# Performance work log

Hardware: AMD Instinct MI355X
Metric: run time of the kernel (lower is better)

## Reference

```python
import jax, jax.numpy as jnp
import numpy as np

B, C, T, H, W = 2, 256, 16, 32, 32
NH = 8
GROUPS = 32
EPS = 1e-6


def setup_inputs() -> dict:
    key = jax.random.key(0)
    ks = jax.random.split(key, 10)
    r = lambda k, shape: jax.random.normal(k, shape, dtype=jnp.float32) * 0.02
    return dict(
        x=jax.random.normal(ks[0], (B, C, T, H, W), dtype=jnp.float32),
        gn_gamma=jnp.ones((C,), jnp.float32),
        gn_beta=jnp.zeros((C,), jnp.float32),
        wq_s=r(ks[1], (C, C)), bq_s=jnp.zeros((C,), jnp.float32),
        wk_s=r(ks[2], (C, C)), bk_s=jnp.zeros((C,), jnp.float32),
        wv_s=r(ks[3], (C, C)), bv_s=jnp.zeros((C,), jnp.float32),
        wo_s=r(ks[4], (C, C)), bo_s=jnp.zeros((C,), jnp.float32),
        wq_t=r(ks[5], (C, C)),
        wk_t=r(ks[6], (C, C)),
        wv_t=r(ks[7], (C, C)),
        wf_t=r(ks[8], (C, C)), bf_t=jnp.zeros((C,), jnp.float32),
    )


def group_norm(x, gamma, beta):
    # x: (N, C, H, W), GroupNorm(32, eps=1e-6, affine)
    n, c, h, w = x.shape
    xg = x.reshape(n, GROUPS, c // GROUPS, h, w)
    mu = xg.mean(axis=(2, 3, 4), keepdims=True)
    var = xg.var(axis=(2, 3, 4), keepdims=True)
    xg = (xg - mu) * jax.lax.rsqrt(var + EPS)
    return xg.reshape(n, c, h, w) * gamma[None, :, None, None] + beta[None, :, None, None]


def spatial_attention(x, gn_gamma, gn_beta, wq, bq, wk, bk, wv, bv, wo, bo):
    # ldm SpatialSelfAttention: norm -> 1x1 conv q/k/v -> full HW self-attn -> 1x1 proj -> residual
    n, c, h, w = x.shape
    hf = group_norm(x, gn_gamma, gn_beta).reshape(n, c, h * w)  # (N, C, HW)
    q = jnp.einsum('oc,bcn->bno', wq, hf) + bq                  # (N, HW, C)
    k = jnp.einsum('oc,bcn->bon', wk, hf) + bk[None, :, None]   # (N, C, HW)
    v = jnp.einsum('oc,bcn->bon', wv, hf) + bv[None, :, None]   # (N, C, HW)
    attn = jax.nn.softmax(jnp.einsum('bic,bcj->bij', q, k) * (c ** -0.5), axis=-1)  # (N, HW, HW)
    out = jnp.einsum('bcj,bij->bci', v, attn)                   # (N, C, HW)
    out = jnp.einsum('oc,bcn->bon', wo, out) + bo[None, :, None]
    return x + out.reshape(n, c, h, w)


def axial_temporal_attention(x, wq, wk, wv, wf, bf):
    # x: (B, T, H, W, C); VideoGPT MultiHeadAttention with AxialAttention over T (axial_dim=-4)
    b, t, h, w, c = x.shape
    dk = c // NH

    def heads(y):  # (B,T,H,W,C) -> (B,H,W,NH,T,dk)
        return jnp.transpose(y.reshape(b, t, h, w, NH, dk), (0, 2, 3, 4, 1, 5))

    q = heads(x @ wq)
    k = heads(x @ wk)
    v = heads(x @ wv)
    scores = jnp.einsum('bhwntd,bhwnsd->bhwnts', q, k) / jnp.sqrt(jnp.float32(dk))
    attn = jax.nn.softmax(scores, axis=-1)
    out = jnp.einsum('bhwnts,bhwnsd->bhwntd', attn, v)          # (B,H,W,NH,T,dk)
    out = jnp.transpose(out, (0, 4, 1, 2, 3, 5)).reshape(b, t, h, w, c)
    return out @ wf + bf


def reference(x, gn_gamma, gn_beta, wq_s, bq_s, wk_s, bk_s, wv_s, bv_s, wo_s, bo_s,
              wq_t, wk_t, wv_t, wf_t, bf_t):
    b, c, t, h, w = x.shape
    # spatial branch: torch does a raw reshape (B,C,T,H,W)->(B*T,C,H,W); replicate exactly
    s = spatial_attention(x.reshape(b * t, c, h, w), gn_gamma, gn_beta,
                          wq_s, bq_s, wk_s, bk_s, wv_s, bv_s, wo_s, bo_s)
    s = s.reshape(b, c, t, h, w)
    # temporal branch: channels-last, axial attention over T
    xt = jnp.moveaxis(x, 1, -1)                                 # (B,T,H,W,C)
    tt = axial_temporal_attention(xt, wq_t, wk_t, wv_t, wf_t, bf_t)
    return s + jnp.moveaxis(tt, -1, 1)
```

## Files before the change

kernel.cpp:

```cpp
#include <hip/hip_runtime.h>
#include <stdint.h>

typedef uint16_t u16;
typedef __attribute__((ext_vector_type(8))) short s8v;
typedef __attribute__((ext_vector_type(4))) float f32x4;
typedef __attribute__((ext_vector_type(16))) float f32x16;
typedef __attribute__((ext_vector_type(4))) unsigned short us4;
typedef __attribute__((ext_vector_type(4))) unsigned int u32x4;

__device__ __forceinline__ float bf2f(u16 u) {
  union { uint32_t i; float f; } x; x.i = ((uint32_t)u) << 16; return x.f;
}
__device__ __forceinline__ u16 f2bf(float f) {
  union { float f; uint32_t i; } x; x.f = f;
  uint32_t r = (x.i + 0x7FFFu + ((x.i >> 16) & 1u)) >> 16;
  return (u16)r;
}
__device__ __forceinline__ uint32_t cvtpk(float a, float b) {
  uint32_t r;
  asm("v_cvt_pk_bf16_f32 %0, %1, %2" : "=v"(r) : "v"(a), "v"(b));
  return r;
}
__device__ __forceinline__ void gl2lds16(const u16* g, u16* l) {
  __builtin_amdgcn_global_load_lds(
      (const __attribute__((address_space(1))) uint32_t*)g,
      (__attribute__((address_space(3))) uint32_t*)l, 16, 0, 0);
}

__global__ __launch_bounds__(256) void gn_stats_kernel(const float* __restrict__ x,
                                                       float2* __restrict__ stats) {
  const int tid = threadIdx.x;
  const float* p = x + (long)blockIdx.x * 8192;
  float s = 0.f, s2 = 0.f;
#pragma unroll
  for (int it = 0; it < 8; ++it) {
    float4 v = *(const float4*)(p + it * 1024 + tid * 4);
    s  += v.x + v.y + v.z + v.w;
    s2 += v.x * v.x + v.y * v.y + v.z * v.z + v.w * v.w;
  }
#pragma unroll
  for (int off = 32; off >= 1; off >>= 1) {
    s  += __shfl_down(s, off);
    s2 += __shfl_down(s2, off);
  }
  __shared__ float ps[4], ps2[4];
  const int wv = tid >> 6, lane = tid & 63;
  if (lane == 0) { ps[wv] = s; ps2[wv] = s2; }
  __syncthreads();
  if (tid == 0) {
    float S1 = ps[0] + ps[1] + ps[2] + ps[3];
    float S2 = ps2[0] + ps2[1] + ps2[2] + ps2[3];
    float mean = S1 * (1.f / 8192.f);
    float var = S2 * (1.f / 8192.f) - mean * mean;
    stats[blockIdx.x] = make_float2(mean, rsqrtf(var + 1e-6f));
  }
}

__global__ __launch_bounds__(256) void wprep_kernel(
    const float* __restrict__ s0, const float* __restrict__ s1,
    const float* __restrict__ s2, const float* __restrict__ s3,
    const float* __restrict__ s4, const float* __restrict__ s5,
    const float* __restrict__ s6, const float* __restrict__ s7,
    u16* __restrict__ wbf) {
  const int mat = blockIdx.x, rb = blockIdx.y;
  const float* src = mat==0?s0:mat==1?s1:mat==2?s2:mat==3?s3:mat==4?s4:mat==5?s5:mat==6?s6:s7;
  u16* dst = wbf + mat * 65536 + rb * 16384;
  const int tid = threadIdx.x;
  if (mat < 4) {
    const float* sb = src + rb * 16384;
#pragma unroll
    for (int it = 0; it < 16; ++it) {
      int idx = it * 256 + tid;
      float4 v = *(const float4*)(sb + idx * 4);
      us4 o; o[0]=f2bf(v.x); o[1]=f2bf(v.y); o[2]=f2bf(v.z); o[3]=f2bf(v.w);
      *(us4*)(dst + idx * 4) = o;
    }
  } else {
    __shared__ u16 tl[64][264];
#pragma unroll
    for (int it = 0; it < 16; ++it) {
      int idx = it * 256 + tid;
      int c = idx >> 4, o4 = idx & 15;
      float4 v = *(const float4*)(src + c * 256 + rb * 64 + o4 * 4);
      tl[o4*4+0][c] = f2bf(v.x);
      tl[o4*4+1][c] = f2bf(v.y);
      tl[o4*4+2][c] = f2bf(v.z);
      tl[o4*4+3][c] = f2bf(v.w);
    }
    __syncthreads();
#pragma unroll
    for (int it = 0; it < 16; ++it) {
      int idx = it * 256 + tid;
      int o = idx >> 6, c4 = idx & 63;
      us4 u;
#pragma unroll
      for (int j = 0; j < 4; ++j) u[j] = tl[o][c4*4+j];
      *(us4*)(dst + o * 256 + c4 * 4) = u;
    }
  }
}

__global__ __launch_bounds__(512) void qkvst_kernel(
    const float* __restrict__ x, const float2* __restrict__ stats,
    const float* __restrict__ gamma, const float* __restrict__ beta,
    const u16* __restrict__ wbf,
    const float* __restrict__ bq, const float* __restrict__ bk, const float* __restrict__ bv,
    u16* __restrict__ qb, u16* __restrict__ kb, u16* __restrict__ vb,
    u16* __restrict__ qt, u16* __restrict__ kt, u16* __restrict__ vt) {
  __shared__ float gas[256], bes[256];
  __shared__ u16 ALDS[128 * 256];
  __shared__ u16 WLDS[2][64 * 256];
  const int bid = blockIdx.x;
  const int b = bid >> 7, st = bid & 127;
  const int s0 = st * 128;
  const int tt = s0 >> 10;
  const int n = b * 16 + tt;
  const int p0 = s0 & 1023;
  const long bbase = (long)b * 4194304;
  const long nbase = (long)n * 262144;
  const int tid = threadIdx.x, w = tid >> 6, lane = tid & 63;
  const int lhi = lane >> 4, llo = lane & 15;

  if (tid < 256) {
    float2 stv = stats[n * 32 + (tid >> 3)];
    float ga = gamma[tid] * stv.y;
    gas[tid] = ga;
    bes[tid] = beta[tid] - stv.x * ga;
  }
  const float* xb = x + bbase + s0;
#pragma unroll
  for (int it = 0; it < 16; ++it) {
    int idx = it * 512 + tid;
    int p = idx & 127, c4 = idx >> 7;
    us4 o;
#pragma unroll
    for (int j = 0; j < 4; ++j)
      o[j] = f2bf(xb[(long)(c4 * 4 + j) * 16384 + p]);
    int ch = c4 >> 1;
    *(us4*)&ALDS[p * 256 + ((ch ^ (p & 7)) << 3) + ((c4 & 1) << 2)] = o;
  }
  __syncthreads();
  const int arow = w * 16 + llo;
  s8v ar[8], ag[8];
#pragma unroll
  for (int kk = 0; kk < 8; ++kk)
    ar[kk] = *(const s8v*)&ALDS[arow * 256 + (((kk * 4 + lhi) ^ (arow & 7)) << 3)];
#pragma unroll
  for (int kk = 0; kk < 8; ++kk) {
    const int cb = kk * 32 + lhi * 8;
    s8v gg;
#pragma unroll
    for (int j = 0; j < 8; ++j)
      gg[j] = (short)f2bf(bf2f((u16)ar[kk][j]) * gas[cb + j] + bes[cb + j]);
    ag[kk] = gg;
  }

  auto stageW4 = [&](int t, int bu) {
    const int mat = (t < 12) ? (t >> 2) : (4 + ((t - 12) >> 2));
    const int sub = (t < 12) ? (t & 3) : ((t - 12) & 3);
    const u16* wsrc = wbf + mat * 65536 + (long)sub * 16384;
#pragma unroll
    for (int ii = 0; ii < 4; ++ii) {
      int s = ii * 512 + tid;
      int row = s >> 5, ch = s & 31;
      gl2lds16(wsrc + row * 256 + ((ch ^ (row & 7)) << 3), &WLDS[bu][s * 8]);
    }
  };

  stageW4(0, 0);
  __syncthreads();

  u16* vtl = ALDS;
  for (int t = 0; t < 24; ++t) {
    const int cur = t & 1;
    if (t < 23) stageW4(t + 1, cur ^ 1);
    f32x4 acc[4] = {};
    if (t < 12) {
#pragma unroll
      for (int kk = 0; kk < 8; ++kk)
#pragma unroll
        for (int nf = 0; nf < 4; ++nf) {
          int row = nf * 16 + llo;
          s8v bfr = *(const s8v*)&WLDS[cur][row * 256 + (((kk * 4 + lhi) ^ (row & 7)) << 3)];
          acc[nf] = __builtin_amdgcn_mfma_f32_16x16x32_bf16(ag[kk], bfr, acc[nf], 0, 0, 0);
        }
    } else {
#pragma unroll
      for (int kk = 0; kk < 8; ++kk)
#pragma unroll
        for (int nf = 0; nf < 4; ++nf) {
          int row = nf * 16 + llo;
          s8v bfr = *(const s8v*)&WLDS[cur][row * 256 + (((kk * 4 + lhi) ^ (row & 7)) << 3)];
          acc[nf] = __builtin_amdgcn_mfma_f32_16x16x32_bf16(ar[kk], bfr, acc[nf], 0, 0, 0);
        }
    }
    const int o0 = ((t < 12) ? (t & 3) : ((t - 12) & 3)) * 64;
    if (t < 8) {
      u16* dstb = (t < 4) ? qb : kb;
      const float* bias = (t < 4) ? bq : bk;
#pragma unroll
      for (int nf = 0; nf < 4; ++nf) {
        int o = o0 + nf * 16 + llo;
        float b_ = bias[o];
#pragma unroll
        for (int r = 0; r < 4; ++r)
          dstb[nbase + (long)(p0 + w * 16 + lhi * 4 + r) * 256 + o] = f2bf(acc[nf][r] + b_);
      }
    } else if (t < 12) {
#pragma unroll
      for (int nf = 0; nf < 4; ++nf) {
        int o = nf * 16 + llo;
        float b_ = bv[o0 + o];
#pragma unroll
        for (int r = 0; r < 4; ++r)
          vtl[o * 136 + w * 16 + lhi * 4 + r] = f2bf(acc[nf][r] + b_);
      }
      __syncthreads();
#pragma unroll
      for (int ii = 0; ii < 4; ++ii) {
        int i = ii * 512 + tid;
        int o = i >> 5, p4 = (i & 31) * 4;
        us4 u;
#pragma unroll
        for (int j = 0; j < 4; ++j) u[j] = vtl[o * 136 + p4 + j];
        *(us4*)(vb + nbase + (long)(o0 + o) * 1024 + p0 + p4) = u;
      }
    } else {
      u16* dstb = (t < 16) ? qt : (t < 20) ? kt : vt;
#pragma unroll
      for (int nf = 0; nf < 4; ++nf) {
        int o = o0 + nf * 16 + llo;
#pragma unroll
        for (int r = 0; r < 4; ++r)
          dstb[bbase + (long)(s0 + w * 16 + lhi * 4 + r) * 256 + o] = f2bf(acc[nf][r]);
      }
    }
    __syncthreads();
  }
}

__global__ __launch_bounds__(256, 1) void flash_kernel(const u16* __restrict__ qb,
                                                       const u16* __restrict__ kb,
                                                       const u16* __restrict__ vb,
                                                       u16* __restrict__ attb) {
  const int wg = blockIdx.x;
  const int swz = (wg & 7) * 64 + (wg >> 3);
  const int n = swz >> 4, qt = swz & 15;
  const int tid = threadIdx.x, w = tid >> 6, lane = tid & 63;
  const int q5 = lane & 31, h = lane >> 5;
  const int wq = w & 1;
  const int kh = w >> 1;
  const long nbase = (long)n * 262144;

  __shared__ u16 Kb[64 * 256];
  __shared__ u16 Vb[256 * 64];
  __shared__ float2 mlbuf[64];

  const int qrow = qt * 64 + wq * 32 + q5;
  const u16* qr = qb + nbase + (long)qrow * 256 + h * 8;
  s8v qa[16];
#pragma unroll
  for (int kk = 0; kk < 16; ++kk) qa[kk] = *(const s8v*)(qr + kk * 16);

  f32x16 oaccT[8] = {};
  float m_ = -3.4e38f, l_ = 0.f;
  constexpr float CEXP = 0.09016844f;

  auto stageKV = [&](int jt2) {
    const u16* kbase = kb + nbase + (long)jt2 * 16384;
    const u16* vbase = vb + nbase + (long)jt2 * 64;
#pragma unroll
    for (int ii = 0; ii < 8; ++ii) {
      int s = ii * 256 + tid;
      int row = s >> 5, ch = s & 31;
      gl2lds16(kbase + (long)row * 256 + ((ch ^ (row & 7)) << 3), &Kb[s * 8]);
    }
#pragma unroll
    for (int ii = 0; ii < 8; ++ii) {
      int s = ii * 256 + tid;
      int c = s >> 3, ch = s & 7;
      gl2lds16(vbase + (long)c * 1024 + ((ch ^ (c & 7)) << 3), &Vb[s * 8]);
    }
  };

  const int krow = kh * 32 + q5;
  for (int jt = 0; jt < 16; ++jt) {
    stageKV(jt);
    __syncthreads();

    f32x16 sacc = {};
    __builtin_amdgcn_s_setprio(1);
#pragma unroll
    for (int kk = 0; kk < 16; ++kk) {
      s8v kfr = *(const s8v*)&Kb[krow * 256 + (((kk * 2 + h) ^ (krow & 7)) << 3)];
      sacc = __builtin_amdgcn_mfma_f32_32x32x16_bf16(kfr, qa[kk], sacc, 0, 0, 0);
    }
    __builtin_amdgcn_s_setprio(0);
    float tm[8];
#pragma unroll
    for (int r = 0; r < 8; ++r) tm[r] = fmaxf(sacc[2 * r], sacc[2 * r + 1]);
#pragma unroll
    for (int r = 0; r < 4; ++r) tm[r] = fmaxf(tm[r], tm[r + 4]);
    float pm = fmaxf(fmaxf(tm[0], tm[1]), fmaxf(tm[2], tm[3]));
    pm = fmaxf(pm, __shfl_xor(pm, 32));
    if (!__all(pm <= m_ + 128.f)) {
      float scf = exp2f((m_ - pm) * CEXP);
      l_ *= scf;
#pragma unroll
      for (int cf = 0; cf < 8; ++cf)
#pragma unroll
        for (int r = 0; r < 16; ++r) oaccT[cf][r] *= scf;
      m_ = pm;
    }
#pragma unroll
    for (int r = 0; r < 16; ++r) sacc[r] = exp2f((sacc[r] - m_) * CEXP);
    float ts[8];
#pragma unroll
    for (int r = 0; r < 8; ++r) ts[r] = sacc[2 * r] + sacc[2 * r + 1];
#pragma unroll
    for (int r = 0; r < 4; ++r) ts[r] = ts[r] + ts[r + 4];
    float rs = (ts[0] + ts[1]) + (ts[2] + ts[3]);
    rs += __shfl_xor(rs, 32);
    l_ += rs;
    uint32_t pk[4][2];
#pragma unroll
    for (int g = 0; g < 4; ++g) {
      pk[g][0] = cvtpk(sacc[4 * g + 0], sacc[4 * g + 1]);
      pk[g][1] = cvtpk(sacc[4 * g + 2], sacc[4 * g + 3]);
    }
#pragma unroll
    for (int js = 0; js < 2; ++js) {
      uint32_t own0 = pk[2 * js + h][0];
      uint32_t own1 = pk[2 * js + h][1];
      uint32_t snd0 = pk[2 * js + (h ^ 1)][0];
      uint32_t snd1 = pk[2 * js + (h ^ 1)][1];
      uint32_t rcv0 = __shfl_xor(snd0, 32);
      uint32_t rcv1 = __shfl_xor(snd1, 32);
      u32x4 pw;
      pw[0] = h ? rcv0 : own0;
      pw[1] = h ? rcv1 : own1;
      pw[2] = h ? own0 : rcv0;
      pw[3] = h ? own1 : rcv1;
      s8v pa = __builtin_bit_cast(s8v, pw);
      __builtin_amdgcn_s_setprio(1);
#pragma unroll
      for (int cf = 0; cf < 8; ++cf) {
        int c = cf * 32 + q5;
        s8v vfr = *(const s8v*)&Vb[c * 64 + (((kh * 4 + js * 2 + h) ^ (c & 7)) << 3)];
        oaccT[cf] = __builtin_amdgcn_mfma_f32_32x32x16_bf16(vfr, pa, oaccT[cf], 0, 0, 0);
      }
      __builtin_amdgcn_s_setprio(0);
    }
    __syncthreads();
  }
  uint32_t* OH = (uint32_t*)&Vb[0];
  u16* tl = &Kb[0];
  if (kh == 1) {
#pragma unroll
    for (int cf = 0; cf < 8; ++cf)
#pragma unroll
      for (int i = 0; i < 8; ++i)
        OH[(((wq * 8 + cf) * 8 + i) * 2 + h) * 32 + q5] =
            cvtpk(oaccT[cf][2 * i], oaccT[cf][2 * i + 1]);
    if (h == 0) mlbuf[wq * 32 + q5] = make_float2(m_, l_);
  }
  __syncthreads();
  if (kh == 0) {
    float2 pml = mlbuf[wq * 32 + q5];
    float M = fmaxf(m_, pml.x);
    float alo = exp2f((m_ - M) * CEXP);
    float ahi = exp2f((pml.x - M) * CEXP);
    float linv = 1.f / (l_ * alo + pml.y * ahi);
    float slo = alo * linv, shi = ahi * linv;
    const int myq = wq * 32 + q5;
#pragma unroll
    for (int cf = 0; cf < 8; ++cf) {
      float v[16];
#pragma unroll
      for (int i = 0; i < 8; ++i) {
        uint32_t pv = OH[(((wq * 8 + cf) * 8 + i) * 2 + h) * 32 + q5];
        v[2 * i]     = oaccT[cf][2 * i] * slo + bf2f((u16)(pv & 0xffff)) * shi;
        v[2 * i + 1] = oaccT[cf][2 * i + 1] * slo + bf2f((u16)(pv >> 16)) * shi;
      }
#pragma unroll
      for (int g = 0; g < 4; ++g) {
        uint2 val;
        val.x = cvtpk(v[4 * g + 0], v[4 * g + 1]);
        val.y = cvtpk(v[4 * g + 2], v[4 * g + 3]);
        int ch = (cf * 4 + g) ^ (myq & 7);
        *(uint2*)&tl[myq * 256 + ch * 8 + h * 4] = val;
      }
    }
  }
  __syncthreads();
  const int qo = tid >> 2, qu = tid & 3;
  u16* obase = attb + nbase + (long)(qt * 64 + qo) * 256;
#pragma unroll
  for (int u = 0; u < 8; ++u) {
    int c16 = qu * 8 + u;
    u32x4 vv = *(const u32x4*)&tl[qo * 256 + ((c16 ^ (qo & 7)) << 3)];
    *(u32x4*)(obase + c16 * 8) = vv;
  }
}

__global__ __launch_bounds__(256) void tattn_kernel(const u16* __restrict__ qt,
                                                    const u16* __restrict__ kt,
                                                    const u16* __restrict__ vt,
                                                    u16* __restrict__ ot) {
  const int bi = blockIdx.x >> 10, hw = blockIdx.x & 1023;
  const long base = (long)bi * 4194304 + (long)hw * 256;
  __shared__ float qs[16][260], ks[16][260], vs[16][260];
  __shared__ u16 os[16][256];
  const int tid = threadIdx.x;
#pragma unroll
  for (int it = 0; it < 4; ++it) {
    int idx = it * 256 + tid;
    int t = idx >> 6, cv = idx & 63;
    long g = base + (long)t * 262144 + cv * 4;
    us4 a = *(const us4*)(qt + g);
    us4 b = *(const us4*)(kt + g);
    us4 c = *(const us4*)(vt + g);
#pragma unroll
    for (int j = 0; j < 4; ++j) {
      qs[t][cv * 4 + j] = bf2f(a[j]);
      ks[t][cv * 4 + j] = bf2f(b[j]);
      vs[t][cv * 4 + j] = bf2f(c[j]);
    }
  }
  __syncthreads();
  if (tid < 128) {
    const int h = tid >> 4, t = tid & 15;
    const int c0 = h * 32;
    float sc[16];
    float mx = -3.4e38f;
#pragma unroll
    for (int t2 = 0; t2 < 16; ++t2) {
      float d = 0.f;
#pragma unroll
      for (int dd = 0; dd < 32; ++dd) d += qs[t][c0 + dd] * ks[t2][c0 + dd];
      sc[t2] = d * 0.17677669529663687f;
      mx = fmaxf(mx, sc[t2]);
    }
    float sum = 0.f;
#pragma unroll
    for (int t2 = 0; t2 < 16; ++t2) { sc[t2] = __expf(sc[t2] - mx); sum += sc[t2]; }
    float inv = 1.f / sum;
#pragma unroll
    for (int dd = 0; dd < 32; ++dd) {
      float o = 0.f;
#pragma unroll
      for (int t2 = 0; t2 < 16; ++t2) o += sc[t2] * vs[t2][c0 + dd];
      os[t][c0 + dd] = f2bf(o * inv);
    }
  }
  __syncthreads();
#pragma unroll
  for (int it = 0; it < 4; ++it) {
    int idx = it * 256 + tid;
    int t = idx >> 6, cv = idx & 63;
    us4 o4;
#pragma unroll
    for (int j = 0; j < 4; ++j) o4[j] = os[t][cv * 4 + j];
    *(us4*)(ot + base + (long)t * 262144 + cv * 4) = o4;
  }
}

__global__ __launch_bounds__(512) void tfinal_kernel(
    const u16* __restrict__ ott, const u16* __restrict__ wbf,
    u16* __restrict__ tmpT) {
  __shared__ u16 ALDS[128 * 256];
  __shared__ u16 WLDS[2][64 * 256];
  const int bid = blockIdx.x;
  const int b = bid >> 7, st = bid & 127;
  const int s0 = st * 128;
  const int tid = threadIdx.x, w = tid >> 6, lane = tid & 63;
  const int lhi = lane >> 4, llo = lane & 15;
  const long bbase = (long)b * 4194304;

  const u16* otS = ott + bbase + (long)s0 * 256;
#pragma unroll
  for (int ii = 0; ii < 8; ++ii) {
    int i0 = (w * 8 + ii) * 64;
    int g = i0 + lane;
    int row = g >> 5, ch = g & 31;
    gl2lds16(otS + row * 256 + ((ch ^ (row & 7)) << 3), &ALDS[i0 * 8]);
  }
  __syncthreads();
  const int arow = w * 16 + llo;
  s8v qa[8];
#pragma unroll
  for (int kk = 0; kk < 8; ++kk)
    qa[kk] = *(const s8v*)&ALDS[arow * 256 + (((kk * 4 + lhi) ^ (arow & 7)) << 3)];

  auto stageW = [&](int t, int bu) {
    const u16* wsrc = wbf + 7 * 65536 + (long)t * 16384;
#pragma unroll
    for (int ii = 0; ii < 4; ++ii) {
      int i0 = (w * 4 + ii) * 64;
      int g = i0 + lane;
      int row = g >> 5, ch = g & 31;
      gl2lds16(wsrc + row * 256 + ((ch ^ (row & 7)) << 3), &WLDS[bu][i0 * 8]);
    }
  };
  stageW(0, 0);
  __syncthreads();
  u16* vtl = ALDS;
  for (int t = 0; t < 4; ++t) {
    const int cur = t & 1;
    if (t < 3) stageW(t + 1, cur ^ 1);
    f32x4 acc[4] = {};
#pragma unroll
    for (int kk = 0; kk < 8; ++kk)
#pragma unroll
      for (int nf = 0; nf < 4; ++nf) {
        int row = nf * 16 + llo;
        s8v bb = *(const s8v*)&WLDS[cur][row * 256 + (((kk * 4 + lhi) ^ (row & 7)) << 3)];
        acc[nf] = __builtin_amdgcn_mfma_f32_16x16x32_bf16(qa[kk], bb, acc[nf], 0, 0, 0);
      }
#pragma unroll
    for (int nf = 0; nf < 4; ++nf) {
      int o = nf * 16 + llo;
#pragma unroll
      for (int r = 0; r < 4; ++r)
        vtl[o * 136 + w * 16 + lhi * 4 + r] = f2bf(acc[nf][r]);
    }
    __syncthreads();
    const int o0 = t * 64;
#pragma unroll
    for (int ii = 0; ii < 4; ++ii) {
      int i = ii * 512 + tid;
      int o = i >> 5, p4 = (i & 31) * 4;
      us4 uu;
#pragma unroll
      for (int j = 0; j < 4; ++j) uu[j] = vtl[o * 136 + p4 + j];
      *(us4*)(tmpT + bbase + (long)(o0 + o) * 16384 + s0 + p4) = uu;
    }
    __syncthreads();
  }
}

__global__ __launch_bounds__(256) void outproj_kernel(
    const float* __restrict__ x, const u16* __restrict__ attb,
    const u16* __restrict__ tmpT, const u16* __restrict__ wbf,
    const float* __restrict__ bo, const float* __restrict__ bf,
    float* __restrict__ out) {
  __shared__ u16 attL[64 * 256];
  const int u = blockIdx.x;
  const int wkx = (u & 7) * 256 + (u >> 3);
  const int otile = wkx & 3, pt = (wkx >> 2) & 15, n = wkx >> 6;
  const int b = n >> 4;
  const int o0 = otile * 64, p0 = pt * 64;
  const int tid = threadIdx.x, w = tid >> 6, lane = tid & 63;
  const int lhi = lane >> 4, llo = lane & 15;
  const long nbase = (long)n * 262144;

  const u16* attS = attb + nbase + (long)p0 * 256;
#pragma unroll
  for (int ii = 0; ii < 8; ++ii) {
    int i0 = (w * 8 + ii) * 64;
    int g = i0 + lane;
    int row = g >> 5, ch = g & 31;
    gl2lds16(attS + row * 256 + ((ch ^ (row & 7)) << 3), &attL[i0 * 8]);
  }
  const u16* woR = wbf + 3 * 65536 + (long)(o0 + w * 16 + llo) * 256;
  s8v woa[8];
#pragma unroll
  for (int kk = 0; kk < 8; ++kk)
    woa[kk] = *(const s8v*)(woR + kk * 32 + lhi * 8);
  __syncthreads();
  f32x4 acc[4] = {};
#pragma unroll
  for (int kk = 0; kk < 8; ++kk)
#pragma unroll
    for (int nf = 0; nf < 4; ++nf) {
      int row = nf * 16 + llo;
      s8v b1 = *(const s8v*)&attL[row * 256 + (((kk * 4 + lhi) ^ (row & 7)) << 3)];
      acc[nf] = __builtin_amdgcn_mfma_f32_16x16x32_bf16(woa[kk], b1, acc[nf], 0, 0, 0);
    }
#pragma unroll
  for (int r = 0; r < 4; ++r) {
    int cp = o0 + w * 16 + lhi * 4 + r;
    int co = ((n & 15) << 4) + (cp >> 4);
    int tt = cp & 15;
    float bias = bo[cp] + bf[co];
    const u16* tr = tmpT + (long)b * 4194304 + (long)co * 16384 + tt * 1024 + p0;
    const float* xr = x + nbase + (long)cp * 1024 + p0;
    float* orow = out + nbase + (long)cp * 1024 + p0;
#pragma unroll
    for (int nf = 0; nf < 4; ++nf) {
      int p = nf * 16 + llo;
      orow[p] = acc[nf][r] + bias + xr[p] + bf2f(tr[p]);
    }
  }
}

extern "C" void kernel_launch(void* const* d_in, const int* in_sizes, int n_in,
                              void* d_out, int out_size, void* d_ws, size_t ws_size,
                              hipStream_t stream) {
  const float* x     = (const float*)d_in[0];
  const float* gam   = (const float*)d_in[1];
  const float* bet   = (const float*)d_in[2];
  const float* wq_s  = (const float*)d_in[3];
  const float* bq_s  = (const float*)d_in[4];
  const float* wk_s  = (const float*)d_in[5];
  const float* bk_s  = (const float*)d_in[6];
  const float* wv_s  = (const float*)d_in[7];
  const float* bv_s  = (const float*)d_in[8];
  const float* wo_s  = (const float*)d_in[9];
  const float* bo_s  = (const float*)d_in[10];
  const float* wq_t  = (const float*)d_in[11];
  const float* wk_t  = (const float*)d_in[12];
  const float* wv_t  = (const float*)d_in[13];
  const float* wf_t  = (const float*)d_in[14];
  const float* bf_t  = (const float*)d_in[15];
  float* out = (float*)d_out;

  u16* qb   = (u16*)d_ws;
  u16* kb   = qb + 8388608;
  u16* vb   = kb + 8388608;
  u16* attb = vb + 8388608;
  u16* ottb = attb + 8388608;
  u16* wbf  = ottb + 8388608;
  u16* qtb  = wbf + 524288;
  u16* ktb  = qtb + 8388608;
  u16* vtb  = ktb + 8388608;
  float2* stats = (float2*)(vtb + 8388608);
  u16* tmpT = qtb;

  gn_stats_kernel<<<1024, 256, 0, stream>>>(x, stats);
  wprep_kernel<<<dim3(8, 4), 256, 0, stream>>>(wq_s, wk_s, wv_s, wo_s,
                                               wq_t, wk_t, wv_t, wf_t, wbf);
  qkvst_kernel<<<256, 512, 0, stream>>>(x, stats, gam, bet, wbf,
                                        bq_s, bk_s, bv_s, qb, kb, vb, qtb, ktb, vtb);
  flash_kernel<<<512, 256, 0, stream>>>(qb, kb, vb, attb);
  tattn_kernel<<<2048, 256, 0, stream>>>(qtb, ktb, vtb, ottb);
  tfinal_kernel<<<256, 512, 0, stream>>>(ottb, wbf, tmpT);
  outproj_kernel<<<2048, 256, 0, stream>>>(x, attb, tmpT, wbf, bo_s, bf_t, out);
}
```

Before: 239.5 us.

## Double-buffer K/V in flash kernel and give each wave its own 32 query rows

The flash attention kernel now handles 128 query rows per workgroup, one 32-row slice per wave, and each wave covers the full 64-key tile instead of splitting keys between wave pairs. That removes the cross-wave softmax merge through LDS at the end. K/V tiles are double-buffered so the next tile's global-to-LDS load is issued before computing on the current one, which drops one barrier per iteration. The grid halves to 256 workgroups and LDS use doubles, which may lower occupancy and leave some CUs idle.

```diff
diff --git a/kernel.cpp b/kernel.cpp
--- a/kernel.cpp
+++ b/kernel.cpp
@@ -244,19 +244,16 @@
                                                        const u16* __restrict__ vb,
                                                        u16* __restrict__ attb) {
   const int wg = blockIdx.x;
-  const int swz = (wg & 7) * 64 + (wg >> 3);
-  const int n = swz >> 4, qt = swz & 15;
+  const int swz = (wg & 7) * 32 + (wg >> 3);
+  const int n = swz >> 3, qt = swz & 7;
   const int tid = threadIdx.x, w = tid >> 6, lane = tid & 63;
   const int q5 = lane & 31, h = lane >> 5;
-  const int wq = w & 1;
-  const int kh = w >> 1;
   const long nbase = (long)n * 262144;
 
-  __shared__ u16 Kb[64 * 256];
-  __shared__ u16 Vb[256 * 64];
-  __shared__ float2 mlbuf[64];
-
-  const int qrow = qt * 64 + wq * 32 + q5;
+  __shared__ u16 Kb[2][64 * 256];
+  __shared__ u16 Vb[2][256 * 64];
+
+  const int qrow = qt * 128 + w * 32 + q5;
   const u16* qr = qb + nbase + (long)qrow * 256 + h * 8;
   s8v qa[16];
 #pragma unroll
@@ -266,39 +263,47 @@
   float m_ = -3.4e38f, l_ = 0.f;
   constexpr float CEXP = 0.09016844f;
 
-  auto stageKV = [&](int jt2) {
+  auto stageKV = [&](int jt2, int b) {
     const u16* kbase = kb + nbase + (long)jt2 * 16384;
     const u16* vbase = vb + nbase + (long)jt2 * 64;
 #pragma unroll
     for (int ii = 0; ii < 8; ++ii) {
-      int s = ii * 256 + tid;
-      int row = s >> 5, ch = s & 31;
-      gl2lds16(kbase + (long)row * 256 + ((ch ^ (row & 7)) << 3), &Kb[s * 8]);
+      int slot = ii * 256 + tid;
+      int row = slot >> 5, ch = slot & 31;
+      gl2lds16(kbase + (long)row * 256 + ((ch ^ (row & 7)) << 3), &Kb[b][slot * 8]);
     }
 #pragma unroll
     for (int ii = 0; ii < 8; ++ii) {
-      int s = ii * 256 + tid;
-      int c = s >> 3, ch = s & 7;
-      gl2lds16(vbase + (long)c * 1024 + ((ch ^ (c & 7)) << 3), &Vb[s * 8]);
+      int slot = ii * 256 + tid;
+      int c = slot >> 3, ch = slot & 7;
+      gl2lds16(vbase + (long)c * 1024 + ((ch ^ (c & 7)) << 3), &Vb[b][slot * 8]);
     }
   };
 
-  const int krow = kh * 32 + q5;
+  stageKV(0, 0);
+  __syncthreads();
+
   for (int jt = 0; jt < 16; ++jt) {
-    stageKV(jt);
-    __syncthreads();
-
-    f32x16 sacc = {};
+    const int cur = jt & 1;
+    if (jt < 15) stageKV(jt + 1, cur ^ 1);
+
+    f32x16 sacc[2] = {};
     __builtin_amdgcn_s_setprio(1);
 #pragma unroll
     for (int kk = 0; kk < 16; ++kk) {
-      s8v kfr = *(const s8v*)&Kb[krow * 256 + (((kk * 2 + h) ^ (krow & 7)) << 3)];
-      sacc = __builtin_amdgcn_mfma_f32_32x32x16_bf16(kfr, qa[kk], sacc, 0, 0, 0);
+#pragma unroll
+      for (int f = 0; f < 2; ++f) {
+        int krow = f * 32 + q5;
+        s8v kfr = *(const s8v*)&Kb[cur][krow * 256 + (((kk * 2 + h) ^ (q5 & 7)) << 3)];
+        sacc[f] = __builtin_amdgcn_mfma_f32_32x32x16_bf16(kfr, qa[kk], sacc[f], 0, 0, 0);
+      }
     }
     __builtin_amdgcn_s_setprio(0);
-    float tm[8];
-#pragma unroll
-    for (int r = 0; r < 8; ++r) tm[r] = fmaxf(sacc[2 * r], sacc[2 * r + 1]);
+    float tm[16];
+#pragma unroll
+    for (int r = 0; r < 16; ++r) tm[r] = fmaxf(sacc[0][r], sacc[1][r]);
+#pragma unroll
+    for (int r = 0; r < 8; ++r) tm[r] = fmaxf(tm[r], tm[r + 8]);
 #pragma unroll
     for (int r = 0; r < 4; ++r) tm[r] = fmaxf(tm[r], tm[r + 4]);
     float pm = fmaxf(fmaxf(tm[0], tm[1]), fmaxf(tm[2], tm[3]));
@@ -313,27 +318,34 @@
       m_ = pm;
     }
 #pragma unroll
-    for (int r = 0; r < 16; ++r) sacc[r] = exp2f((sacc[r] - m_) * CEXP);
-    float ts[8];
-#pragma unroll
-    for (int r = 0; r < 8; ++r) ts[r] = sacc[2 * r] + sacc[2 * r + 1];
+    for (int f = 0; f < 2; ++f)
+#pragma unroll
+      for (int r = 0; r < 16; ++r) sacc[f][r] = exp2f((sacc[f][r] - m_) * CEXP);
+    float ts[16];
+#pragma unroll
+    for (int r = 0; r < 16; ++r) ts[r] = sacc[0][r] + sacc[1][r];
+#pragma unroll
+    for (int r = 0; r < 8; ++r) ts[r] = ts[r] + ts[r + 8];
 #pragma unroll
     for (int r = 0; r < 4; ++r) ts[r] = ts[r] + ts[r + 4];
     float rs = (ts[0] + ts[1]) + (ts[2] + ts[3]);
     rs += __shfl_xor(rs, 32);
     l_ += rs;
-    uint32_t pk[4][2];
-#pragma unroll
-    for (int g = 0; g < 4; ++g) {
-      pk[g][0] = cvtpk(sacc[4 * g + 0], sacc[4 * g + 1]);
-      pk[g][1] = cvtpk(sacc[4 * g + 2], sacc[4 * g + 3]);
-    }
-#pragma unroll
-    for (int js = 0; js < 2; ++js) {
-      uint32_t own0 = pk[2 * js + h][0];
-      uint32_t own1 = pk[2 * js + h][1];
-      uint32_t snd0 = pk[2 * js + (h ^ 1)][0];
-      uint32_t snd1 = pk[2 * js + (h ^ 1)][1];
+    uint32_t pk[2][4][2];
+#pragma unroll
+    for (int f = 0; f < 2; ++f)
+#pragma unroll
+      for (int g = 0; g < 4; ++g) {
+        pk[f][g][0] = cvtpk(sacc[f][4 * g + 0], sacc[f][4 * g + 1]);
+        pk[f][g][1] = cvtpk(sacc[f][4 * g + 2], sacc[f][4 * g + 3]);
+      }
+#pragma unroll
+    for (int js = 0; js < 4; ++js) {
+      const int f = js >> 1, g0 = 2 * (js & 1);
+      uint32_t own0 = h ? pk[f][g0 + 1][0] : pk[f][g0][0];
+      uint32_t own1 = h ? pk[f][g0 + 1][1] : pk[f][g0][1];
+      uint32_t snd0 = h ? pk[f][g0][0] : pk[f][g0 + 1][0];
+      uint32_t snd1 = h ? pk[f][g0][1] : pk[f][g0 + 1][1];
       uint32_t rcv0 = __shfl_xor(snd0, 32);
       uint32_t rcv1 = __shfl_xor(snd1, 32);
       u32x4 pw;
@@ -346,60 +358,35 @@
 #pragma unroll
       for (int cf = 0; cf < 8; ++cf) {
         int c = cf * 32 + q5;
-        s8v vfr = *(const s8v*)&Vb[c * 64 + (((kh * 4 + js * 2 + h) ^ (c & 7)) << 3)];
+        s8v vfr = *(const s8v*)&Vb[cur][c * 64 + (((js * 2 + h) ^ (c & 7)) << 3)];
         oaccT[cf] = __builtin_amdgcn_mfma_f32_32x32x16_bf16(vfr, pa, oaccT[cf], 0, 0, 0);
       }
       __builtin_amdgcn_s_setprio(0);
     }
     __syncthreads();
   }
-  uint32_t* OH = (uint32_t*)&Vb[0];
-  u16* tl = &Kb[0];
-  if (kh == 1) {
-#pragma unroll
-    for (int cf = 0; cf < 8; ++cf)
-#pragma unroll
-      for (int i = 0; i < 8; ++i)
-        OH[(((wq * 8 + cf) * 8 + i) * 2 + h) * 32 + q5] =
-            cvtpk(oaccT[cf][2 * i], oaccT[cf][2 * i + 1]);
-    if (h == 0) mlbuf[wq * 32 + q5] = make_float2(m_, l_);
-  }
-  __syncthreads();
-  if (kh == 0) {
-    float2 pml = mlbuf[wq * 32 + q5];
-    float M = fmaxf(m_, pml.x);
-    float alo = exp2f((m_ - M) * CEXP);
-    float ahi = exp2f((pml.x - M) * CEXP);
-    float linv = 1.f / (l_ * alo + pml.y * ahi);
-    float slo = alo * linv, shi = ahi * linv;
-    const int myq = wq * 32 + q5;
-#pragma unroll
-    for (int cf = 0; cf < 8; ++cf) {
-      float v[16];
-#pragma unroll
-      for (int i = 0; i < 8; ++i) {
-        uint32_t pv = OH[(((wq * 8 + cf) * 8 + i) * 2 + h) * 32 + q5];
-        v[2 * i]     = oaccT[cf][2 * i] * slo + bf2f((u16)(pv & 0xffff)) * shi;
-        v[2 * i + 1] = oaccT[cf][2 * i + 1] * slo + bf2f((u16)(pv >> 16)) * shi;
-      }
-#pragma unroll
-      for (int g = 0; g < 4; ++g) {
-        uint2 val;
-        val.x = cvtpk(v[4 * g + 0], v[4 * g + 1]);
-        val.y = cvtpk(v[4 * g + 2], v[4 * g + 3]);
-        int ch = (cf * 4 + g) ^ (myq & 7);
-        *(uint2*)&tl[myq * 256 + ch * 8 + h * 4] = val;
-      }
-    }
-  }
-  __syncthreads();
-  const int qo = tid >> 2, qu = tid & 3;
-  u16* obase = attb + nbase + (long)(qt * 64 + qo) * 256;
-#pragma unroll
-  for (int u = 0; u < 8; ++u) {
-    int c16 = qu * 8 + u;
-    u32x4 vv = *(const u32x4*)&tl[qo * 256 + ((c16 ^ (qo & 7)) << 3)];
-    *(u32x4*)(obase + c16 * 8) = vv;
+  float inv = 1.f / l_;
+  u16* tl = &Kb[0][0];
+  __syncthreads();
+  const int myq = w * 32 + q5;
+#pragma unroll
+  for (int cf = 0; cf < 8; ++cf)
+#pragma unroll
+    for (int g = 0; g < 4; ++g) {
+      uint32_t w0 = cvtpk(oaccT[cf][4 * g + 0] * inv, oaccT[cf][4 * g + 1] * inv);
+      uint32_t w1 = cvtpk(oaccT[cf][4 * g + 2] * inv, oaccT[cf][4 * g + 3] * inv);
+      int ch = (cf * 4 + g) ^ (myq & 7);
+      uint2 val; val.x = w0; val.y = w1;
+      *(uint2*)&tl[myq * 256 + ch * 8 + h * 4] = val;
+    }
+  __syncthreads();
+  const int qo = tid >> 1, hr = tid & 1;
+  u16* obase = attb + nbase + (long)(qt * 128 + qo) * 256;
+#pragma unroll
+  for (int u = 0; u < 16; ++u) {
+    int c16 = hr * 16 + u;
+    u32x4 v = *(const u32x4*)&tl[qo * 256 + ((c16 ^ (qo & 7)) << 3)];
+    *(u32x4*)(obase + c16 * 8) = v;
   }
 }
 
@@ -632,7 +619,7 @@
                                                wq_t, wk_t, wv_t, wf_t, wbf);
   qkvst_kernel<<<256, 512, 0, stream>>>(x, stats, gam, bet, wbf,
                                         bq_s, bk_s, bv_s, qb, kb, vb, qtb, ktb, vtb);
-  flash_kernel<<<512, 256, 0, stream>>>(qb, kb, vb, attb);
+  flash_kernel<<<256, 256, 0, stream>>>(qb, kb, vb, attb);
   tattn_kernel<<<2048, 256, 0, stream>>>(qtb, ktb, vtb, ottb);
   tfinal_kernel<<<256, 512, 0, stream>>>(ottb, wbf, tmpT);
   outproj_kernel<<<2048, 256, 0, stream>>>(x, attb, tmpT, wbf, bo_s, bf_t, out);
```

Result: faster. 206.2 us (-13.9%).
